# Performance work log

Hardware: AMD Instinct MI355X
Metric: run time of the kernel (lower is better)

Reference implementation:

```python
import jax, jax.numpy as jnp
import numpy as np

N = 8192
D = 128
AVG_DEG = 32


def setup_inputs() -> dict:
    key = jax.random.key(0)
    ks = jax.random.split(key, 10)
    Z = jax.random.normal(ks[0], (N, D), dtype=jnp.float32)
    # random symmetric binary adjacency with avg degree ~ AVG_DEG
    p = AVG_DEG / N
    adj = (jax.random.uniform(ks[1], (N, N)) < p).astype(jnp.float32)
    adj = jnp.maximum(adj, adj.T)
    # symmetric normalized adjacency: D^{-1/2} A D^{-1/2}
    deg = adj.sum(axis=1)
    d_inv_sqrt = jnp.where(deg > 0, 1.0 / jnp.sqrt(deg), 0.0)
    A_norm = d_inv_sqrt[:, None] * adj * d_inv_sqrt[None, :]
    sc = 1.0 / np.sqrt(D)
    W_D = jax.random.uniform(ks[2], (D, D), minval=-sc, maxval=sc, dtype=jnp.float32)
    W_C = jax.random.uniform(ks[3], (D, D), minval=-sc, maxval=sc, dtype=jnp.float32)
    w_V = jax.random.uniform(ks[4], (D,), minval=-sc, maxval=sc, dtype=jnp.float32)
    W1 = jax.random.uniform(ks[5], (D, D), minval=-sc, maxval=sc, dtype=jnp.float32)
    b1 = jax.random.uniform(ks[6], (D,), minval=-sc, maxval=sc, dtype=jnp.float32)
    W2 = jax.random.uniform(ks[7], (D, D), minval=-sc, maxval=sc, dtype=jnp.float32)
    b2 = jax.random.uniform(ks[8], (D,), minval=-sc, maxval=sc, dtype=jnp.float32)
    omega_logit = jnp.float32(0.0)  # sigmoid -> 0.5
    delta_logit = jnp.float32(0.0)
    return {"Z": Z, "A_norm": A_norm, "W_D": W_D, "W_C": W_C, "w_V": w_V,
            "W1": W1, "b1": b1, "W2": W2, "b2": b2,
            "omega_logit": omega_logit, "delta_logit": delta_logit}


def reference(Z, A_norm, W_D, W_C, w_V, W1, b1, W2, b2, omega_logit, delta_logit):
    omega = jax.nn.sigmoid(omega_logit)
    delta = jax.nn.sigmoid(delta_logit)
    # Diffusion: ReLU(A_norm @ Z @ W_D^T)
    dif = jax.nn.relu(A_norm @ (Z @ W_D.T))  # [N, D]
    # Convection (standard attention). Since W_V is D->1,
    # W_V(z_i - z_j) == s_i - s_j with s = Z @ w_V -> avoid [N,N,D] tensor.
    s = Z @ w_V                                   # [N]
    V_bar = jax.nn.sigmoid(s[:, None] - s[None, :])  # [N, N]
    A = jax.nn.softmax(V_bar, axis=1)                # row-stochastic [N, N]
    con = A @ (Z @ W_C.T)                            # [N, D]
    # Reaction: nonlinear MLP
    rea = jnp.tanh(Z @ W1.T + b1) @ W2.T + b2        # [N, D]
    return omega * dif + (1.0 - omega) * con + delta * rea
```

## Files before the change

### kernel.cpp

```cpp
#include <hip/hip_runtime.h>
#include <hip/hip_bf16.h>
#include <stdint.h>

#define NN 8192
#define DD 128

typedef float f32x4 __attribute__((ext_vector_type(4)));
typedef __bf16 bf16x8 __attribute__((ext_vector_type(8)));
typedef __bf16 bf16x4 __attribute__((ext_vector_type(4)));

__device__ __forceinline__ f32x4 mfma16(bf16x8 a, bf16x8 b, f32x4 c) {
    return __builtin_amdgcn_mfma_f32_16x16x32_bf16(a, b, c, 0, 0, 0);
}

__device__ __forceinline__ bf16x8 pack8(f32x4 lo, f32x4 hi) {
    bf16x8 r;
    r[0] = (__bf16)lo[0]; r[1] = (__bf16)lo[1]; r[2] = (__bf16)lo[2]; r[3] = (__bf16)lo[3];
    r[4] = (__bf16)hi[0]; r[5] = (__bf16)hi[1]; r[6] = (__bf16)hi[2]; r[7] = (__bf16)hi[3];
    return r;
}

__device__ __forceinline__ float fast_sigmoid(float x) {
    return __builtin_amdgcn_rcpf(1.0f + __expf(-x));
}

__global__ __launch_bounds__(256) void k_prep_sE(
    const float* __restrict__ Z, const float* __restrict__ wV, float* __restrict__ E)
{
    const int wid  = threadIdx.x >> 6;
    const int lane = threadIdx.x & 63;
    const int row  = blockIdx.x * 4 + wid;
    float p = Z[row * DD + lane] * wV[lane] + Z[row * DD + 64 + lane] * wV[64 + lane];
    #pragma unroll
    for (int off = 32; off > 0; off >>= 1) p += __shfl_xor(p, off, 64);
    if (lane == 0) E[row] = __expf(p);
}

__global__ __launch_bounds__(256) void k_conv_w(
    const float* __restrict__ W_D, const float* __restrict__ W_C,
    const float* __restrict__ W1, const float* __restrict__ W2,
    __bf16* __restrict__ Wb)
{
    const int t = blockIdx.x * 256 + threadIdx.x;
    const int m = t >> 12, i = t & 4095;
    const float* src = (m == 0) ? W_D : (m == 1) ? W_C : (m == 2) ? W1 : W2;
    const f32x4 v = *(const f32x4*)(src + i * 4);
    bf16x4 b;
    b[0] = (__bf16)v[0]; b[1] = (__bf16)v[1]; b[2] = (__bf16)v[2]; b[3] = (__bf16)v[3];
    *(bf16x4*)(Wb + m * 16384 + i * 4) = b;
}

__global__ __launch_bounds__(256) void k_prep2(
    const float* __restrict__ Z, const __bf16* __restrict__ Wb,
    const float* __restrict__ b1, const float* __restrict__ b2,
    const float* __restrict__ delta_logit,
    __bf16* __restrict__ XB, __bf16* __restrict__ YB, __bf16* __restrict__ REAT)
{
    __shared__ __bf16 Hs[32][136];
    const int tid = threadIdx.x;
    const int w = tid >> 6, l = tid & 63;
    const int lr = l & 15, lg = l >> 4;
    const int wr = w & 1, wn = w >> 1;
    const int r0 = blockIdx.x * 32;
    const int arow = r0 + 16 * wr + lr;
    const __bf16* WDb = Wb;
    const __bf16* WCb = Wb + 16384;
    const __bf16* W1b = Wb + 32768;
    const __bf16* W2b = Wb + 49152;

    const f32x4 zero4 = {0.f, 0.f, 0.f, 0.f};
    f32x4 aXD[4], aY[4], aH[4];
    #pragma unroll
    for (int i = 0; i < 4; ++i) { aXD[i] = zero4; aY[i] = zero4; aH[i] = zero4; }

    #pragma unroll
    for (int t = 0; t < 4; ++t) {
        const int k0 = 32 * t + 8 * lg;
        const bf16x8 af = pack8(*(const f32x4*)(Z + arow * DD + k0),
                                *(const f32x4*)(Z + arow * DD + k0 + 4));
        #pragma unroll
        for (int nf = 0; nf < 4; ++nf) {
            const int col = 64 * wn + 16 * nf + lr;
            aXD[nf] = mfma16(af, *(const bf16x8*)(WDb + col * DD + k0), aXD[nf]);
            aY[nf]  = mfma16(af, *(const bf16x8*)(WCb + col * DD + k0), aY[nf]);
            aH[nf]  = mfma16(af, *(const bf16x8*)(W1b + col * DD + k0), aH[nf]);
        }
    }

    const int orow = r0 + 16 * wr + 4 * lg;
    const int tile = orow >> 5, kin = orow & 31;
    #pragma unroll
    for (int nf = 0; nf < 4; ++nf) {
        const int col = 64 * wn + 16 * nf + lr;
        bf16x4 xo, yo;
        const float bb1 = b1[col];
        #pragma unroll
        for (int r = 0; r < 4; ++r) {
            xo[r] = (__bf16)aXD[nf][r];
            yo[r] = (__bf16)aY[nf][r];
            const float x = aH[nf][r] + bb1;
            const float e = __expf(2.0f * x);
            Hs[16 * wr + 4 * lg + r][col] = (__bf16)(1.0f - 2.0f * __builtin_amdgcn_rcpf(e + 1.0f));
        }
        *(bf16x4*)(XB + tile * 4096 + col * 32 + kin) = xo;
        *(bf16x4*)(YB + tile * 4096 + col * 32 + kin) = yo;
    }
    __syncthreads();

    f32x4 aR[4];
    #pragma unroll
    for (int i = 0; i < 4; ++i) aR[i] = zero4;
    #pragma unroll
    for (int t = 0; t < 4; ++t) {
        const int k0 = 32 * t + 8 * lg;
        const bf16x8 hf = *(const bf16x8*)(&Hs[16 * wr + lr][k0]);
        #pragma unroll
        for (int nf = 0; nf < 4; ++nf) {
            const int col = 64 * wn + 16 * nf + lr;
            aR[nf] = mfma16(hf, *(const bf16x8*)(W2b + col * DD + k0), aR[nf]);
        }
    }
    const float delta = fast_sigmoid(delta_logit[0]);
    #pragma unroll
    for (int nf = 0; nf < 4; ++nf) {
        const int col = 64 * wn + 16 * nf + lr;
        const float bb2 = b2[col];
        bf16x4 ro;
        #pragma unroll
        for (int r = 0; r < 4; ++r) ro[r] = (__bf16)(delta * (aR[nf][r] + bb2));
        *(bf16x4*)(REAT + (size_t)col * NN + orow) = ro;
    }
}

__global__ __launch_bounds__(512, 2) void k_big(
    const float* __restrict__ A, const float* __restrict__ E,
    const __bf16* __restrict__ XB, const __bf16* __restrict__ YB,
    const __bf16* __restrict__ REAT, const float* __restrict__ omega_logit,
    float* __restrict__ out)
{
    __shared__ float red[4][64][36];
    const int tid = threadIdx.x;
    const int wid = tid >> 6, l = tid & 63;
    const int lr = l & 15, lg = l >> 4;
    const int wc = wid & 1, wr = (wid >> 1) & 1, kh = wid >> 2;
    const int r0 = blockIdx.x * 32;
    const int row = r0 + 16 * wr + lr;
    const int colbase = 64 * wc;
    const int kstart = kh * 4096;

    const float* ap = A + (size_t)row * NN + kstart + 8 * lg;
    const float* ep = E + kstart + 8 * lg;
    const __bf16* xp = XB + (size_t)(kstart >> 5) * 4096 + (colbase + lr) * 32 + 8 * lg;
    const __bf16* yp = YB + (size_t)(kstart >> 5) * 4096 + (colbase + lr) * 32 + 8 * lg;
    const float u = E[row];

    const f32x4 zero4 = {0.f, 0.f, 0.f, 0.f};
    f32x4 aD[4], aC[4], aDen = zero4;
    #pragma unroll
    for (int i = 0; i < 4; ++i) { aD[i] = zero4; aC[i] = zero4; }
    bf16x8 ones;
    #pragma unroll
    for (int i = 0; i < 8; ++i) ones[i] = (__bf16)1.0f;

    f32x4 a0A, a1A, e0A, e1A, a0B, a1B, e0B, e1B;
    bf16x8 bxA[4], byA[4], bxB[4], byB[4];
    intptr_t adv = 32;

#define LOADT(S) do {                                                        \
        a0##S = *(const f32x4*)(ap); a1##S = *(const f32x4*)(ap + 4);        \
        e0##S = *(const f32x4*)(ep); e1##S = *(const f32x4*)(ep + 4);        \
        _Pragma("unroll")                                                    \
        for (int c = 0; c < 4; ++c) {                                        \
            bx##S[c] = *(const bf16x8*)(xp + c * 512);                       \
            by##S[c] = *(const bf16x8*)(yp + c * 512);                       \
        }                                                                    \
        ap += adv; ep += adv; xp += adv * 128; yp += adv * 128;              \
    } while (0)

#define COMPT(S) do {                                                        \
        bf16x8 gf;                                                           \
        _Pragma("unroll")                                                    \
        for (int j = 0; j < 4; ++j) {                                        \
            gf[j]     = (__bf16)__expf(u * __builtin_amdgcn_rcpf(u + e0##S[j])); \
            gf[4 + j] = (__bf16)__expf(u * __builtin_amdgcn_rcpf(u + e1##S[j])); \
        }                                                                    \
        const bf16x8 af = pack8(a0##S, a1##S);                               \
        _Pragma("unroll")                                                    \
        for (int c = 0; c < 4; ++c) {                                        \
            aD[c] = mfma16(af, bx##S[c], aD[c]);                             \
            aC[c] = mfma16(gf, by##S[c], aC[c]);                             \
        }                                                                    \
        aDen = mfma16(gf, ones, aDen);                                       \
    } while (0)

    LOADT(A);
    for (int it = 0; it < 64; ++it) {
        if (it == 63) adv = 0;
        LOADT(B);
        COMPT(A);
        LOADT(A);
        COMPT(B);
    }
#undef LOADT
#undef COMPT

    const int grp = wr * 2 + wc;
    if (kh == 1) {
        float* slot = &red[grp][l][0];
        #pragma unroll
        for (int c = 0; c < 4; ++c) {
            *(f32x4*)(slot + 4 * c)      = aD[c];
            *(f32x4*)(slot + 16 + 4 * c) = aC[c];
        }
        *(f32x4*)(slot + 32) = aDen;
    }
    __syncthreads();
    if (kh == 0) {
        const float* slot = &red[grp][l][0];
        #pragma unroll
        for (int c = 0; c < 4; ++c) {
            aD[c] += *(const f32x4*)(slot + 4 * c);
            aC[c] += *(const f32x4*)(slot + 16 + 4 * c);
        }
        aDen += *(const f32x4*)(slot + 32);

        const float omega = fast_sigmoid(omega_logit[0]);
        const float om1 = 1.0f - omega;
        const int rbase = r0 + 16 * wr + 4 * lg;
        #pragma unroll
        for (int c = 0; c < 4; ++c) {
            const int col = colbase + 16 * c + lr;
            const bf16x4 rea4 = *(const bf16x4*)(REAT + (size_t)col * NN + rbase);
            #pragma unroll
            for (int r = 0; r < 4; ++r) {
                const float dv = fmaxf(aD[c][r], 0.0f);
                const float cv = aC[c][r] * __builtin_amdgcn_rcpf(aDen[r]);
                out[(size_t)(rbase + r) * DD + col] = (float)rea4[r] + omega * dv + om1 * cv;
            }
        }
    }
}

extern "C" void kernel_launch(void* const* d_in, const int* in_sizes, int n_in,
                              void* d_out, int out_size, void* d_ws, size_t ws_size,
                              hipStream_t stream) {
    (void)in_sizes; (void)n_in; (void)out_size; (void)ws_size;
    const float* Z   = (const float*)d_in[0];
    const float* A   = (const float*)d_in[1];
    const float* W_D = (const float*)d_in[2];
    const float* W_C = (const float*)d_in[3];
    const float* wV  = (const float*)d_in[4];
    const float* W1  = (const float*)d_in[5];
    const float* b1  = (const float*)d_in[6];
    const float* W2  = (const float*)d_in[7];
    const float* b2  = (const float*)d_in[8];
    const float* omega_logit = (const float*)d_in[9];
    const float* delta_logit = (const float*)d_in[10];
    float* out = (float*)d_out;

    float*  E    = (float*)d_ws;
    __bf16* Wb   = (__bf16*)((char*)d_ws + 32768);
    __bf16* XB   = (__bf16*)((char*)d_ws + 262144);
    __bf16* YB   = (__bf16*)((char*)d_ws + 262144 + 2097152);
    __bf16* REAT = (__bf16*)((char*)d_ws + 262144 + 2 * 2097152);

    k_prep_sE<<<dim3(2048), dim3(256), 0, stream>>>(Z, wV, E);
    k_conv_w<<<dim3(64), dim3(256), 0, stream>>>(W_D, W_C, W1, W2, Wb);
    k_prep2<<<dim3(256), dim3(256), 0, stream>>>(Z, Wb, b1, b2, delta_logit, XB, YB, REAT);
    k_big<<<dim3(256), dim3(512), 0, stream>>>(A, E, XB, YB, REAT, omega_logit, out);
}
```

Before: 538.7 us.

## Split k_big waves over output columns instead of K halves, deepen prefetch

After: 581.1 us. 7.9% more time.

```diff
diff --git a/kernel.cpp b/kernel.cpp
--- a/kernel.cpp
+++ b/kernel.cpp
@@ -132,111 +132,85 @@
     }
 }
 
-__global__ __launch_bounds__(512, 2) void k_big(
+__global__ __launch_bounds__(512) __attribute__((amdgpu_waves_per_eu(2, 2))) void k_big(
     const float* __restrict__ A, const float* __restrict__ E,
     const __bf16* __restrict__ XB, const __bf16* __restrict__ YB,
     const __bf16* __restrict__ REAT, const float* __restrict__ omega_logit,
     float* __restrict__ out)
 {
-    __shared__ float red[4][64][36];
     const int tid = threadIdx.x;
     const int wid = tid >> 6, l = tid & 63;
     const int lr = l & 15, lg = l >> 4;
-    const int wc = wid & 1, wr = (wid >> 1) & 1, kh = wid >> 2;
+    const int wc = wid & 3, wr = wid >> 2;
     const int r0 = blockIdx.x * 32;
     const int row = r0 + 16 * wr + lr;
-    const int colbase = 64 * wc;
-    const int kstart = kh * 4096;
-
-    const float* ap = A + (size_t)row * NN + kstart + 8 * lg;
-    const float* ep = E + kstart + 8 * lg;
-    const __bf16* xp = XB + (size_t)(kstart >> 5) * 4096 + (colbase + lr) * 32 + 8 * lg;
-    const __bf16* yp = YB + (size_t)(kstart >> 5) * 4096 + (colbase + lr) * 32 + 8 * lg;
+    const int colbase = 32 * wc;
+
+    const float* ap = A + (size_t)row * NN + 8 * lg;
+    const float* ep = E + 8 * lg;
+    const __bf16* xp = XB + (colbase + lr) * 32 + 8 * lg;
+    const __bf16* yp = YB + (colbase + lr) * 32 + 8 * lg;
     const float u = E[row];
 
     const f32x4 zero4 = {0.f, 0.f, 0.f, 0.f};
-    f32x4 aD[4], aC[4], aDen = zero4;
-    #pragma unroll
-    for (int i = 0; i < 4; ++i) { aD[i] = zero4; aC[i] = zero4; }
+    f32x4 aD0 = zero4, aD1 = zero4, aC0 = zero4, aC1 = zero4, aDen = zero4;
     bf16x8 ones;
     #pragma unroll
     for (int i = 0; i < 8; ++i) ones[i] = (__bf16)1.0f;
 
-    f32x4 a0A, a1A, e0A, e1A, a0B, a1B, e0B, e1B;
-    bf16x8 bxA[4], byA[4], bxB[4], byB[4];
-    intptr_t adv = 32;
+    f32x4 a0_0, a1_0, e0_0, e1_0; bf16x8 bx0_0, bx1_0, by0_0, by1_0;
+    f32x4 a0_1, a1_1, e0_1, e1_1; bf16x8 bx0_1, bx1_1, by0_1, by1_1;
+    f32x4 a0_2, a1_2, e0_2, e1_2; bf16x8 bx0_2, bx1_2, by0_2, by1_2;
+    f32x4 a0_3, a1_3, e0_3, e1_3; bf16x8 bx0_3, bx1_3, by0_3, by1_3;
 
 #define LOADT(S) do {                                                        \
-        a0##S = *(const f32x4*)(ap); a1##S = *(const f32x4*)(ap + 4);        \
-        e0##S = *(const f32x4*)(ep); e1##S = *(const f32x4*)(ep + 4);        \
-        _Pragma("unroll")                                                    \
-        for (int c = 0; c < 4; ++c) {                                        \
-            bx##S[c] = *(const bf16x8*)(xp + c * 512);                       \
-            by##S[c] = *(const bf16x8*)(yp + c * 512);                       \
-        }                                                                    \
-        ap += adv; ep += adv; xp += adv * 128; yp += adv * 128;              \
+        a0_##S = *(const f32x4*)(ap); a1_##S = *(const f32x4*)(ap + 4);      \
+        e0_##S = *(const f32x4*)(ep); e1_##S = *(const f32x4*)(ep + 4);      \
+        bx0_##S = *(const bf16x8*)(xp);        bx1_##S = *(const bf16x8*)(xp + 512); \
+        by0_##S = *(const bf16x8*)(yp);        by1_##S = *(const bf16x8*)(yp + 512); \
+        ap += 32; ep += 32; xp += 4096; yp += 4096;                          \
     } while (0)
 
 #define COMPT(S) do {                                                        \
         bf16x8 gf;                                                           \
         _Pragma("unroll")                                                    \
         for (int j = 0; j < 4; ++j) {                                        \
-            gf[j]     = (__bf16)__expf(u * __builtin_amdgcn_rcpf(u + e0##S[j])); \
-            gf[4 + j] = (__bf16)__expf(u * __builtin_amdgcn_rcpf(u + e1##S[j])); \
+            gf[j]     = (__bf16)__expf(u * __builtin_amdgcn_rcpf(u + e0_##S[j])); \
+            gf[4 + j] = (__bf16)__expf(u * __builtin_amdgcn_rcpf(u + e1_##S[j])); \
         }                                                                    \
-        const bf16x8 af = pack8(a0##S, a1##S);                               \
-        _Pragma("unroll")                                                    \
-        for (int c = 0; c < 4; ++c) {                                        \
-            aD[c] = mfma16(af, bx##S[c], aD[c]);                             \
-            aC[c] = mfma16(gf, by##S[c], aC[c]);                             \
-        }                                                                    \
+        const bf16x8 af = pack8(a0_##S, a1_##S);                             \
+        aD0 = mfma16(af, bx0_##S, aD0);                                      \
+        aD1 = mfma16(af, bx1_##S, aD1);                                      \
+        aC0 = mfma16(gf, by0_##S, aC0);                                      \
+        aC1 = mfma16(gf, by1_##S, aC1);                                      \
         aDen = mfma16(gf, ones, aDen);                                       \
     } while (0)
 
-    LOADT(A);
-    for (int it = 0; it < 64; ++it) {
-        if (it == 63) adv = 0;
-        LOADT(B);
-        COMPT(A);
-        LOADT(A);
-        COMPT(B);
-    }
+    LOADT(0); LOADT(1); LOADT(2); LOADT(3);
+    for (int it = 0; it < 63; ++it) {
+        COMPT(0); LOADT(0);
+        COMPT(1); LOADT(1);
+        COMPT(2); LOADT(2);
+        COMPT(3); LOADT(3);
+    }
+    COMPT(0); COMPT(1); COMPT(2); COMPT(3);
 #undef LOADT
 #undef COMPT
 
-    const int grp = wr * 2 + wc;
-    if (kh == 1) {
-        float* slot = &red[grp][l][0];
-        #pragma unroll
-        for (int c = 0; c < 4; ++c) {
-            *(f32x4*)(slot + 4 * c)      = aD[c];
-            *(f32x4*)(slot + 16 + 4 * c) = aC[c];
-        }
-        *(f32x4*)(slot + 32) = aDen;
-    }
-    __syncthreads();
-    if (kh == 0) {
-        const float* slot = &red[grp][l][0];
-        #pragma unroll
-        for (int c = 0; c < 4; ++c) {
-            aD[c] += *(const f32x4*)(slot + 4 * c);
-            aC[c] += *(const f32x4*)(slot + 16 + 4 * c);
-        }
-        aDen += *(const f32x4*)(slot + 32);
-
-        const float omega = fast_sigmoid(omega_logit[0]);
-        const float om1 = 1.0f - omega;
-        const int rbase = r0 + 16 * wr + 4 * lg;
-        #pragma unroll
-        for (int c = 0; c < 4; ++c) {
-            const int col = colbase + 16 * c + lr;
-            const bf16x4 rea4 = *(const bf16x4*)(REAT + (size_t)col * NN + rbase);
-            #pragma unroll
-            for (int r = 0; r < 4; ++r) {
-                const float dv = fmaxf(aD[c][r], 0.0f);
-                const float cv = aC[c][r] * __builtin_amdgcn_rcpf(aDen[r]);
-                out[(size_t)(rbase + r) * DD + col] = (float)rea4[r] + omega * dv + om1 * cv;
-            }
+    const float omega = fast_sigmoid(omega_logit[0]);
+    const float om1 = 1.0f - omega;
+    const int rbase = r0 + 16 * wr + 4 * lg;
+    #pragma unroll
+    for (int c = 0; c < 2; ++c) {
+        const f32x4 ad = c ? aD1 : aD0;
+        const f32x4 ac = c ? aC1 : aC0;
+        const int col = colbase + 16 * c + lr;
+        const bf16x4 rea4 = *(const bf16x4*)(REAT + (size_t)col * NN + rbase);
+        #pragma unroll
+        for (int r = 0; r < 4; ++r) {
+            const float dv = fmaxf(ad[r], 0.0f);
+            const float cv = ac[r] * __builtin_amdgcn_rcpf(aDen[r]);
+            out[(size_t)(rbase + r) * DD + col] = (float)rea4[r] + omega * dv + om1 * cv;
         }
     }
 }
```
